# Kernel tuning notes

Hardware: AMD Instinct MI355X
Metric: run time of the kernel (lower is better)

## Reference

```python
import jax, jax.numpy as jnp
import numpy as np

N_HEAD = 16
MASK_NEG = -10000.0


def setup_inputs() -> dict:
    key = jax.random.key(0)
    k1, k2, k3 = jax.random.split(key, 3)
    B, S, D = 4, 2048, 1024
    x = jax.random.normal(k1, (B, S, D), dtype=jnp.float32)
    c_attn_w = jax.random.normal(k2, (D, 3 * D), dtype=jnp.float32) * 0.02
    c_attn_b = jnp.zeros((3 * D,), dtype=jnp.float32)
    c_proj_w = jax.random.normal(k3, (D, D), dtype=jnp.float32) * 0.02
    c_proj_b = jnp.zeros((D,), dtype=jnp.float32)
    return {"x": x, "c_attn_w": c_attn_w, "c_attn_b": c_attn_b,
            "c_proj_w": c_proj_w, "c_proj_b": c_proj_b}


def reference(x, c_attn_w, c_attn_b, c_proj_w, c_proj_b):
    B, S, D = x.shape
    H = N_HEAD
    Dh = D // H
    # fused QKV projection (Conv1D = x @ W + b)
    qkv = x @ c_attn_w + c_attn_b          # [B,S,3D]
    q, k, v = jnp.split(qkv, 3, axis=-1)   # each [B,S,D]
    # split heads -> [B,H,S,Dh]
    q = q.reshape(B, S, H, Dh).transpose(0, 2, 1, 3)
    k = k.reshape(B, S, H, Dh).transpose(0, 2, 1, 3)
    v = v.reshape(B, S, H, Dh).transpose(0, 2, 1, 3)
    # scores with scaling (scale=True)
    w = jnp.einsum('bhqd,bhkd->bhqk', q, k) / jnp.sqrt(jnp.float32(Dh))
    # multiplicative causal mask: w*b + -10000*(1-b)
    b = jnp.tril(jnp.ones((S, S), dtype=w.dtype))[None, None]  # [1,1,S,S]
    w = w * b + MASK_NEG * (1.0 - b)
    w = jax.nn.softmax(w, axis=-1)
    # dropout is identity at inference
    a = jnp.einsum('bhqk,bhkd->bhqd', w, v)  # [B,H,S,Dh]
    a = a.transpose(0, 2, 1, 3).reshape(B, S, D)  # merge heads
    out = a @ c_proj_w + c_proj_b
    return out
```

## Files before the change

### kernel.cpp

```cpp
#include <hip/hip_runtime.h>

typedef unsigned short u16;
typedef short bf16x8 __attribute__((ext_vector_type(8)));
typedef float f32x4 __attribute__((ext_vector_type(4)));
typedef unsigned int u32;
typedef u32 u32x4 __attribute__((ext_vector_type(4)));

#define B_ 4
#define S_ 2048
#define D_ 1024
#define H_ 16
#define DH_ 64
#define M_ 8192
#define SCL2E 0.1803368801111244f

__device__ __forceinline__ u16 f2b(float f) {
  union { float f; unsigned int u; } v; v.f = f;
  unsigned int u = v.u;
  unsigned int r = (u + 0x7FFFu + ((u >> 16) & 1u)) >> 16;
  return (u16)r;
}

__device__ __forceinline__ void gload16(const void* g, void* l) {
  __builtin_amdgcn_global_load_lds(
      (const __attribute__((address_space(1))) unsigned int*)g,
      (__attribute__((address_space(3))) unsigned int*)l,
      16, 0, 0);
}

__device__ __forceinline__ u32 cvt_pk_bf16(float lo, float hi) {
  u32 r;
  asm("v_cvt_pk_bf16_f32 %0, %1, %2" : "=v"(r) : "v"(lo), "v"(hi));
  return r;
}

struct __attribute__((aligned(8))) u16x4 { u16 x, y, z, w; };

__global__ void cvt_f32_bf16(const float* __restrict__ in, u16* __restrict__ out, int n) {
  int i = (blockIdx.x * blockDim.x + threadIdx.x) * 4;
  if (i >= n) return;
  float4 v = *(const float4*)(in + i);
  u16x4 o; o.x = f2b(v.x); o.y = f2b(v.y); o.z = f2b(v.z); o.w = f2b(v.w);
  *(u16x4*)(out + i) = o;
}

__global__ void transpose_cvt(const float* __restrict__ in, u16* __restrict__ out, int R, int C) {
  __shared__ float tile[32][33];
  int c0 = blockIdx.x * 32, r0 = blockIdx.y * 32;
  int tx = threadIdx.x, ty = threadIdx.y;
#pragma unroll
  for (int j = 0; j < 32; j += 8)
    tile[ty + j][tx] = in[(size_t)(r0 + ty + j) * C + c0 + tx];
  __syncthreads();
#pragma unroll
  for (int j = 0; j < 32; j += 8)
    out[(size_t)(c0 + ty + j) * R + r0 + tx] = f2b(tile[tx][ty + j]);
}

template <int MODE>
__global__ __launch_bounds__(256) void gemm_bt(
    const u16* __restrict__ A, const u16* __restrict__ BT,
    const float* __restrict__ bias, float* __restrict__ outf,
    u16* __restrict__ qb, u16* __restrict__ kb, u16* __restrict__ vtb,
    int Ncols, int Kdim) {
  __shared__ __attribute__((aligned(16))) u16 lsA[2][128 * 64];
  __shared__ __attribute__((aligned(16))) u16 lsB[2][128 * 64];
  const int t = threadIdx.x;
  const int lane = t & 63, w = t >> 6;
  const int lhi = lane >> 4, llo = lane & 15;

  const int gx = gridDim.x;
  const int lin = blockIdx.y * gx + blockIdx.x;
  const int nwg = gx * gridDim.y;
  const int sw = (lin & 7) * (nwg >> 3) + (lin >> 3);
  const int m0 = (sw / gx) * 128, n0 = (sw % gx) * 128;

  const int wr = (w >> 1) * 64, wc = (w & 1) * 64;

  const int r8 = lane >> 3;
  const int scolE = ((lane & 7) ^ r8) * 8;
  const int srow = w * 32 + r8;

  f32x4 acc[4][4] = {};
  const int nt = Kdim >> 6;

#define STAGE_G(buf, kk0)                                                        \
  _Pragma("unroll") for (int j = 0; j < 4; ++j) {                                \
    gload16(A + (size_t)(m0 + srow + j * 8) * Kdim + (kk0) + scolE,              \
            &lsA[buf][(w * 32 + j * 8) * 64]);                                   \
    gload16(BT + (size_t)(n0 + srow + j * 8) * Kdim + (kk0) + scolE,             \
            &lsB[buf][(w * 32 + j * 8) * 64]);                                   \
  }

  STAGE_G(0, 0)

  for (int tt = 0; tt < nt; ++tt) {
    const int cur = tt & 1;
    if (tt + 1 < nt) {
      STAGE_G(cur ^ 1, (tt + 1) << 6)
      asm volatile("s_waitcnt vmcnt(8)" ::: "memory");
    } else {
      asm volatile("s_waitcnt vmcnt(0)" ::: "memory");
    }
    __builtin_amdgcn_sched_barrier(0);
    __builtin_amdgcn_s_barrier();
    __builtin_amdgcn_sched_barrier(0);
#pragma unroll
    for (int kk = 0; kk < 2; ++kk) {
      bf16x8 af[4], bfr[4];
#pragma unroll
      for (int i = 0; i < 4; ++i) {
        int ra = wr + i * 16 + llo;
        af[i] = *(const bf16x8*)((const char*)&lsA[cur][ra * 64] +
                                 ((kk * 64 + lhi * 16) ^ ((ra & 7) << 4)));
        int rb = wc + i * 16 + llo;
        bfr[i] = *(const bf16x8*)((const char*)&lsB[cur][rb * 64] +
                                  ((kk * 64 + lhi * 16) ^ ((rb & 7) << 4)));
      }
#pragma unroll
      for (int mi = 0; mi < 4; ++mi)
#pragma unroll
        for (int ni = 0; ni < 4; ++ni)
          acc[mi][ni] = __builtin_amdgcn_mfma_f32_16x16x32_bf16(af[mi], bfr[ni], acc[mi][ni], 0, 0, 0);
    }
    __builtin_amdgcn_sched_barrier(0);
    __builtin_amdgcn_s_barrier();
  }
#undef STAGE_G

  if (MODE == 0) {
#pragma unroll
    for (int mi = 0; mi < 4; ++mi)
#pragma unroll
      for (int ni = 0; ni < 4; ++ni)
#pragma unroll
        for (int r = 0; r < 4; ++r) {
          int m = m0 + wr + mi * 16 + lhi * 4 + r;
          int n = n0 + wc + ni * 16 + llo;
          outf[(size_t)m * Ncols + n] = acc[mi][ni][r] + bias[n];
        }
  } else if (n0 < 1024) {
#pragma unroll
    for (int mi = 0; mi < 4; ++mi)
#pragma unroll
      for (int ni = 0; ni < 4; ++ni)
#pragma unroll
        for (int r = 0; r < 4; ++r) {
          int m = m0 + wr + mi * 16 + lhi * 4 + r;
          int n = n0 + wc + ni * 16 + llo;
          int bidx = m >> 11, s = m & 2047, hh = n >> 6, dh = n & 63;
          qb[((size_t)(bidx * 16 + hh) * 2048 + s) * 64 + dh] =
              f2b((acc[mi][ni][r] + bias[n]) * SCL2E);
        }
  } else if (n0 < 2048) {
#pragma unroll
    for (int mi = 0; mi < 4; ++mi)
#pragma unroll
      for (int ni = 0; ni < 4; ++ni)
#pragma unroll
        for (int r = 0; r < 4; ++r) {
          int m = m0 + wr + mi * 16 + lhi * 4 + r;
          int n2 = n0 - 1024 + wc + ni * 16 + llo;
          int bidx = m >> 11, s = m & 2047, hh = n2 >> 6, dh = n2 & 63;
          kb[((size_t)(bidx * 16 + hh) * 2048 + s) * 64 + dh] =
              f2b(acc[mi][ni][r] + bias[n0 + wc + ni * 16 + llo]);
        }
  } else {
#pragma unroll
    for (int mi = 0; mi < 4; ++mi)
#pragma unroll
      for (int ni = 0; ni < 4; ++ni)
#pragma unroll
        for (int r = 0; r < 4; ++r) {
          int m = m0 + wr + mi * 16 + lhi * 4 + r;
          int n2 = n0 - 2048 + wc + ni * 16 + llo;
          int bidx = m >> 11, s = m & 2047, hh = n2 >> 6, dh = n2 & 63;
          int col = (s & ~127) | ((s & 15) * 8 + ((s >> 4) & 7));
          vtb[((size_t)(bidx * 16 + hh) * 64 + dh) * 2048 + col] =
              f2b(acc[mi][ni][r] + bias[n0 + wc + ni * 16 + llo]);
        }
  }
}

__global__ __launch_bounds__(512) void attn128(
    const u16* __restrict__ Qb, const u16* __restrict__ Kb,
    const u16* __restrict__ VTb, u16* __restrict__ AO) {
  __shared__ __attribute__((aligned(16))) u16 kls[128 * 64];
  __shared__ __attribute__((aligned(16))) u16 vls[64 * 128];
  __shared__ __attribute__((aligned(16))) u16 pl[8][16][136];
  const int t = threadIdx.x, w = t >> 6, lane = t & 63;
  const int lhi = lane >> 4, llo = lane & 15;

  const int lin = blockIdx.y * 8 + blockIdx.x;
  const int bh = ((lin >> 6) << 3) | (lin & 7);
  const int pr = (lin >> 3) & 7;
  const int bb = bh >> 4, hh = bh & 15;

  const u16* Qp = Qb + (size_t)bh * (S_ * DH_);
  const u16* Kp = Kb + (size_t)bh * (S_ * DH_);
  const u16* Vp = VTb + (size_t)bh * (DH_ * S_);

  bf16x8 ones;
#pragma unroll
  for (int i = 0; i < 8; ++i) ones[i] = (short)0x3F80;

  int krow[2], kcolE[2], kdst[2], vrow[2], vcolE[2], vdst[2];
#pragma unroll
  for (int c = 0; c < 2; ++c) {
    int b = c * 8192 + t * 16;
    krow[c] = b >> 7;
    kcolE[c] = (b & 127) >> 1;
    kdst[c] = krow[c] * 128 + ((b & 127) ^ ((krow[c] & 7) << 4));
    vrow[c] = b >> 8;
    vcolE[c] = (b & 255) >> 1;
    vdst[c] = vrow[c] * 256 + ((b & 255) ^ ((vrow[c] & 15) << 4));
  }

  for (int ci = 0; ci < 2; ++ci) {
    const int qc = ci ? (15 - pr) : pr;
    const int q0 = qc * 128;
    const int qrow = q0 + w * 16 + llo;
    bf16x8 aq0 = *(const bf16x8*)(Qp + (size_t)qrow * DH_ + lhi * 8);
    bf16x8 aq1 = *(const bf16x8*)(Qp + (size_t)qrow * DH_ + 32 + lhi * 8);
    const int n128 = qc + 1;

    bf16x8 kst[2], vst[2];
#pragma unroll
    for (int c = 0; c < 2; ++c) {
      kst[c] = *(const bf16x8*)(Kp + (size_t)krow[c] * DH_ + kcolE[c]);
      vst[c] = *(const bf16x8*)(Vp + (size_t)vrow[c] * S_ + vcolE[c]);
    }
    __syncthreads();
#pragma unroll
    for (int c = 0; c < 2; ++c) {
      *(bf16x8*)((char*)kls + kdst[c]) = kst[c];
      *(bf16x8*)((char*)vls + vdst[c]) = vst[c];
    }
    __syncthreads();

    f32x4 o[4] = {};
    f32x4 osum = {};
    const int crow = q0 + w * 16 + lhi * 4;
    const int sw = (llo & 7) << 4;

    for (int tt = 0; tt < n128 - 1; ++tt) {
      const int kv0 = tt << 7;

#pragma unroll
      for (int c = 0; c < 2; ++c) {
        kst[c] = *(const bf16x8*)(Kp + (size_t)(kv0 + 128 + krow[c]) * DH_ + kcolE[c]);
        vst[c] = *(const bf16x8*)(Vp + (size_t)vrow[c] * S_ + kv0 + 128 + vcolE[c]);
      }

      f32x4 sc[8] = {};
      __builtin_amdgcn_s_setprio(1);
#pragma unroll
      for (int f = 0; f < 8; ++f) {
        const char* base = (const char*)kls + (f * 16 + llo) * 128;
        bf16x8 bk0 = *(const bf16x8*)(base + ((lhi * 16) ^ sw));
        bf16x8 bk1 = *(const bf16x8*)(base + ((64 + lhi * 16) ^ sw));
        sc[f] = __builtin_amdgcn_mfma_f32_16x16x32_bf16(aq0, bk0, sc[f], 0, 0, 0);
        sc[f] = __builtin_amdgcn_mfma_f32_16x16x32_bf16(aq1, bk1, sc[f], 0, 0, 0);
      }
      __builtin_amdgcn_s_setprio(0);

#pragma unroll
      for (int r = 0; r < 4; ++r) {
        float p[8];
#pragma unroll
        for (int f = 0; f < 8; ++f) p[f] = exp2f(sc[f][r]);
        u32x4 pw;
        pw[0] = cvt_pk_bf16(p[0], p[1]);
        pw[1] = cvt_pk_bf16(p[2], p[3]);
        pw[2] = cvt_pk_bf16(p[4], p[5]);
        pw[3] = cvt_pk_bf16(p[6], p[7]);
        *(u32x4*)((char*)&pl[w][lhi * 4 + r][0] + llo * 16) = pw;
      }

      __builtin_amdgcn_s_setprio(1);
#pragma unroll
      for (int kk = 0; kk < 4; ++kk) {
        bf16x8 ap = *(const bf16x8*)((const char*)&pl[w][llo][0] + kk * 64 + lhi * 16);
#pragma unroll
        for (int f = 0; f < 4; ++f) {
          const char* vbase = (const char*)vls + (f * 16 + llo) * 256;
          bf16x8 bv = *(const bf16x8*)(vbase + ((kk * 64 + lhi * 16) ^ (llo << 4)));
          o[f] = __builtin_amdgcn_mfma_f32_16x16x32_bf16(ap, bv, o[f], 0, 0, 0);
        }
        osum = __builtin_amdgcn_mfma_f32_16x16x32_bf16(ap, ones, osum, 0, 0, 0);
      }
      __builtin_amdgcn_s_setprio(0);

      __syncthreads();
#pragma unroll
      for (int c = 0; c < 2; ++c) {
        *(bf16x8*)((char*)kls + kdst[c]) = kst[c];
        *(bf16x8*)((char*)vls + vdst[c]) = vst[c];
      }
      __syncthreads();
    }

    {
      const int kv0 = (n128 - 1) << 7;
      f32x4 sc[8] = {};
      __builtin_amdgcn_s_setprio(1);
#pragma unroll
      for (int f = 0; f < 8; ++f) {
        const char* base = (const char*)kls + (f * 16 + llo) * 128;
        bf16x8 bk0 = *(const bf16x8*)(base + ((lhi * 16) ^ sw));
        bf16x8 bk1 = *(const bf16x8*)(base + ((64 + lhi * 16) ^ sw));
        sc[f] = __builtin_amdgcn_mfma_f32_16x16x32_bf16(aq0, bk0, sc[f], 0, 0, 0);
        sc[f] = __builtin_amdgcn_mfma_f32_16x16x32_bf16(aq1, bk1, sc[f], 0, 0, 0);
      }
      __builtin_amdgcn_s_setprio(0);

#pragma unroll
      for (int r = 0; r < 4; ++r) {
        float p[8];
#pragma unroll
        for (int f = 0; f < 8; ++f) {
          float x = sc[f][r];
          if (kv0 + f * 16 + llo > crow + r) x = -1e30f;
          p[f] = exp2f(x);
        }
        u32x4 pw;
        pw[0] = cvt_pk_bf16(p[0], p[1]);
        pw[1] = cvt_pk_bf16(p[2], p[3]);
        pw[2] = cvt_pk_bf16(p[4], p[5]);
        pw[3] = cvt_pk_bf16(p[6], p[7]);
        *(u32x4*)((char*)&pl[w][lhi * 4 + r][0] + llo * 16) = pw;
      }

      __builtin_amdgcn_s_setprio(1);
#pragma unroll
      for (int kk = 0; kk < 4; ++kk) {
        bf16x8 ap = *(const bf16x8*)((const char*)&pl[w][llo][0] + kk * 64 + lhi * 16);
#pragma unroll
        for (int f = 0; f < 4; ++f) {
          const char* vbase = (const char*)vls + (f * 16 + llo) * 256;
          bf16x8 bv = *(const bf16x8*)(vbase + ((kk * 64 + lhi * 16) ^ (llo << 4)));
          o[f] = __builtin_amdgcn_mfma_f32_16x16x32_bf16(ap, bv, o[f], 0, 0, 0);
        }
        osum = __builtin_amdgcn_mfma_f32_16x16x32_bf16(ap, ones, osum, 0, 0, 0);
      }
      __builtin_amdgcn_s_setprio(0);
    }

#pragma unroll
    for (int f = 0; f < 4; ++f)
#pragma unroll
      for (int r = 0; r < 4; ++r) {
        int row = crow + r;
        int dh = f * 16 + llo;
        float val = o[f][r] / osum[r];
        AO[((size_t)bb * S_ + row) * D_ + hh * DH_ + dh] = f2b(val);
      }
  }
}

extern "C" void kernel_launch(void* const* d_in, const int* in_sizes, int n_in,
                              void* d_out, int out_size, void* d_ws, size_t ws_size,
                              hipStream_t stream) {
  const float* x  = (const float*)d_in[0];
  const float* w1 = (const float*)d_in[1];
  const float* b1 = (const float*)d_in[2];
  const float* w2 = (const float*)d_in[3];
  const float* b2 = (const float*)d_in[4];
  float* out = (float*)d_out;
  char* ws = (char*)d_ws;

  u16* xb  = (u16*)(ws);
  u16* w1t = (u16*)(ws + 16777216);
  u16* w2t = (u16*)(ws + 23068672);
  u16* qb  = (u16*)(ws + 25165824);
  u16* kb  = (u16*)(ws + 41943040);
  u16* vtb = (u16*)(ws + 58720256);
  u16* ao  = xb;

  cvt_f32_bf16<<<8192, 256, 0, stream>>>(x, xb, M_ * D_);
  transpose_cvt<<<dim3(96, 32), dim3(32, 8), 0, stream>>>(w1, w1t, 1024, 3072);
  transpose_cvt<<<dim3(32, 32), dim3(32, 8), 0, stream>>>(w2, w2t, 1024, 1024);

  gemm_bt<1><<<dim3(24, 64), 256, 0, stream>>>(xb, w1t, b1, nullptr, qb, kb, vtb, 3072, 1024);
  attn128<<<dim3(8, 64), 512, 0, stream>>>(qb, kb, vtb, ao);
  gemm_bt<0><<<dim3(8, 64), 256, 0, stream>>>(ao, w2t, b2, out, nullptr, nullptr, nullptr, 1024, 1024);
}
```

Measured before the change: 185.5 us.

## Replace QKV GEMM with 256x256-tile 8-wave kernel with phased LDS pipelining

Adds a new gemm256 kernel for the QKV projection that uses 256x256 output tiles with 512 threads, double-buffered LDS, and a four-phase schedule interleaving global-to-LDS loads with MFMA work. Workgroup indices are swizzled across XCD-sized groups for L2 locality. The aim is higher arithmetic intensity and better overlap of memory traffic with compute than the 128x128 gemm_bt path. In exchange, the grid shrinks to 384 blocks at one block per CU, which may leave some CUs idle or unbalanced and raises register pressure.

```diff
diff --git a/kernel.cpp b/kernel.cpp
--- a/kernel.cpp
+++ b/kernel.cpp
@@ -139,45 +139,137 @@
           int n = n0 + wc + ni * 16 + llo;
           outf[(size_t)m * Ncols + n] = acc[mi][ni][r] + bias[n];
         }
-  } else if (n0 < 1024) {
-#pragma unroll
-    for (int mi = 0; mi < 4; ++mi)
-#pragma unroll
-      for (int ni = 0; ni < 4; ++ni)
+  }
+}
+
+__global__ __launch_bounds__(512, 1) void gemm256(
+    const u16* __restrict__ A, const u16* __restrict__ BT,
+    const float* __restrict__ bias,
+    u16* __restrict__ qb, u16* __restrict__ kb, u16* __restrict__ vtb,
+    int Kdim) {
+  __shared__ __attribute__((aligned(16))) u16 lsA[2][2][128 * 64];
+  __shared__ __attribute__((aligned(16))) u16 lsB[2][2][128 * 64];
+  const int t = threadIdx.x;
+  const int lane = t & 63, w = t >> 6;
+  const int lhi = lane >> 4, llo = lane & 15;
+
+  const int gx = gridDim.x;
+  const int lin = blockIdx.y * gx + blockIdx.x;
+  const int nwg = gx * gridDim.y;
+  const int sw = (lin & 7) * (nwg >> 3) + (lin >> 3);
+  const int m0 = (sw / gx) * 256, n0 = (sw % gx) * 256;
+
+  const int wr = w >> 2, wc = w & 3;
+  const int srowj = t >> 3;
+  const int scol = ((t & 7) ^ (srowj & 7)) * 8;
+  const u16* gA = A + (size_t)m0 * Kdim;
+  const u16* gB = BT + (size_t)n0 * Kdim;
+
+  f32x4 acc[8][4] = {};
+  const int nt = Kdim >> 6;
+
+#define STG256(buf, h, kk0)                                                     \
+  { const u16* gp = ((h) < 2 ? gA + (size_t)((h) * 128) * Kdim                  \
+                             : gB + (size_t)(((h) - 2) * 128) * Kdim);          \
+    u16* lp = ((h) < 2 ? &lsA[buf][(h)][0] : &lsB[buf][(h) - 2][0]);            \
+    _Pragma("unroll") for (int j = 0; j < 2; ++j)                               \
+      gload16(gp + (size_t)(j * 64 + srowj) * Kdim + (kk0) + scol,              \
+              lp + j * 4096 + w * 512); }
+
+  STG256(0, 0, 0) STG256(0, 1, 0) STG256(0, 2, 0) STG256(0, 3, 0)
+
+  bf16x8 af[4][2], bfr[2][2];
+
+#define RDA256(c, mh)                                                            \
+  _Pragma("unroll") for (int mi = 0; mi < 4; ++mi)                               \
+  _Pragma("unroll") for (int kk = 0; kk < 2; ++kk) {                             \
+    int rih = (mh) * 64 + mi * 16 + llo;                                         \
+    af[mi][kk] = *(const bf16x8*)((const char*)&lsA[c][wr][0] + rih * 128 +      \
+                                  ((kk * 64 + lhi * 16) ^ ((rih & 7) << 4)));    \
+  }
+#define RDB256(c, nh)                                                            \
+  _Pragma("unroll") for (int ni = 0; ni < 2; ++ni)                               \
+  _Pragma("unroll") for (int kk = 0; kk < 2; ++kk) {                             \
+    int rih = (wc & 1) * 64 + (nh) * 32 + ni * 16 + llo;                         \
+    bfr[ni][kk] = *(const bf16x8*)((const char*)&lsB[c][wc >> 1][0] + rih * 128 +\
+                                   ((kk * 64 + lhi * 16) ^ ((rih & 7) << 4)));   \
+  }
+#define MFMA256(mh, nh)                                                          \
+  __builtin_amdgcn_s_setprio(1);                                                 \
+  _Pragma("unroll") for (int kk = 0; kk < 2; ++kk)                               \
+  _Pragma("unroll") for (int mi = 0; mi < 4; ++mi)                               \
+  _Pragma("unroll") for (int ni = 0; ni < 2; ++ni)                               \
+    acc[(mh) * 4 + mi][(nh) * 2 + ni] = __builtin_amdgcn_mfma_f32_16x16x32_bf16( \
+        af[mi][kk], bfr[ni][kk], acc[(mh) * 4 + mi][(nh) * 2 + ni], 0, 0, 0);    \
+  __builtin_amdgcn_s_setprio(0);
+#define PH_SYNC(cnt)                                                             \
+  asm volatile("s_waitcnt vmcnt(" #cnt ")" ::: "memory");                        \
+  __builtin_amdgcn_sched_barrier(0);                                             \
+  __builtin_amdgcn_s_barrier();                                                  \
+  __builtin_amdgcn_sched_barrier(0);
+
+  for (int kt = 0; kt < nt - 1; ++kt) {
+    const int c = kt & 1, o = c ^ 1;
+    const int kn = (kt + 1) << 6;
+    PH_SYNC(6) RDA256(c, 0) RDB256(c, 0) STG256(o, 0, kn) MFMA256(0, 0)
+    PH_SYNC(6) RDB256(c, 1)              STG256(o, 1, kn) MFMA256(0, 1)
+    PH_SYNC(6) RDA256(c, 1)              STG256(o, 2, kn) MFMA256(1, 1)
+    PH_SYNC(6) RDB256(c, 0)              STG256(o, 3, kn) MFMA256(1, 0)
+  }
+  {
+    const int c = (nt - 1) & 1;
+    PH_SYNC(6) RDA256(c, 0) RDB256(c, 0) MFMA256(0, 0)
+    PH_SYNC(4) RDB256(c, 1)              MFMA256(0, 1)
+    PH_SYNC(2) RDA256(c, 1)              MFMA256(1, 1)
+    PH_SYNC(0) RDB256(c, 0)              MFMA256(1, 0)
+  }
+#undef STG256
+#undef RDA256
+#undef RDB256
+#undef MFMA256
+#undef PH_SYNC
+
+  if (n0 < 1024) {
+#pragma unroll
+    for (int MI = 0; MI < 8; ++MI)
+#pragma unroll
+      for (int NI = 0; NI < 4; ++NI)
 #pragma unroll
         for (int r = 0; r < 4; ++r) {
-          int m = m0 + wr + mi * 16 + lhi * 4 + r;
-          int n = n0 + wc + ni * 16 + llo;
+          int m = m0 + wr * 128 + MI * 16 + lhi * 4 + r;
+          int n = n0 + wc * 64 + NI * 16 + llo;
           int bidx = m >> 11, s = m & 2047, hh = n >> 6, dh = n & 63;
           qb[((size_t)(bidx * 16 + hh) * 2048 + s) * 64 + dh] =
-              f2b((acc[mi][ni][r] + bias[n]) * SCL2E);
+              f2b((acc[MI][NI][r] + bias[n]) * SCL2E);
         }
   } else if (n0 < 2048) {
 #pragma unroll
-    for (int mi = 0; mi < 4; ++mi)
-#pragma unroll
-      for (int ni = 0; ni < 4; ++ni)
+    for (int MI = 0; MI < 8; ++MI)
+#pragma unroll
+      for (int NI = 0; NI < 4; ++NI)
 #pragma unroll
         for (int r = 0; r < 4; ++r) {
-          int m = m0 + wr + mi * 16 + lhi * 4 + r;
-          int n2 = n0 - 1024 + wc + ni * 16 + llo;
+          int m = m0 + wr * 128 + MI * 16 + lhi * 4 + r;
+          int n = n0 + wc * 64 + NI * 16 + llo;
+          int n2 = n - 1024;
           int bidx = m >> 11, s = m & 2047, hh = n2 >> 6, dh = n2 & 63;
           kb[((size_t)(bidx * 16 + hh) * 2048 + s) * 64 + dh] =
-              f2b(acc[mi][ni][r] + bias[n0 + wc + ni * 16 + llo]);
+              f2b(acc[MI][NI][r] + bias[n]);
         }
   } else {
 #pragma unroll
-    for (int mi = 0; mi < 4; ++mi)
-#pragma unroll
-      for (int ni = 0; ni < 4; ++ni)
+    for (int MI = 0; MI < 8; ++MI)
+#pragma unroll
+      for (int NI = 0; NI < 4; ++NI)
 #pragma unroll
         for (int r = 0; r < 4; ++r) {
-          int m = m0 + wr + mi * 16 + lhi * 4 + r;
-          int n2 = n0 - 2048 + wc + ni * 16 + llo;
+          int m = m0 + wr * 128 + MI * 16 + lhi * 4 + r;
+          int n = n0 + wc * 64 + NI * 16 + llo;
+          int n2 = n - 2048;
           int bidx = m >> 11, s = m & 2047, hh = n2 >> 6, dh = n2 & 63;
           int col = (s & ~127) | ((s & 15) * 8 + ((s >> 4) & 7));
           vtb[((size_t)(bidx * 16 + hh) * 64 + dh) * 2048 + col] =
-              f2b(acc[mi][ni][r] + bias[n0 + wc + ni * 16 + llo]);
+              f2b(acc[MI][NI][r] + bias[n]);
         }
   }
 }
@@ -245,7 +337,6 @@
 
     for (int tt = 0; tt < n128 - 1; ++tt) {
       const int kv0 = tt << 7;
-
 #pragma unroll
       for (int c = 0; c < 2; ++c) {
         kst[c] = *(const bf16x8*)(Kp + (size_t)(kv0 + 128 + krow[c]) * DH_ + kcolE[c]);
@@ -381,7 +472,7 @@
   transpose_cvt<<<dim3(96, 32), dim3(32, 8), 0, stream>>>(w1, w1t, 1024, 3072);
   transpose_cvt<<<dim3(32, 32), dim3(32, 8), 0, stream>>>(w2, w2t, 1024, 1024);
 
-  gemm_bt<1><<<dim3(24, 64), 256, 0, stream>>>(xb, w1t, b1, nullptr, qb, kb, vtb, 3072, 1024);
+  gemm256<<<dim3(12, 32), 512, 0, stream>>>(xb, w1t, b1, qb, kb, vtb, 1024);
   attn128<<<dim3(8, 64), 512, 0, stream>>>(qb, kb, vtb, ao);
   gemm_bt<0><<<dim3(8, 64), 256, 0, stream>>>(ao, w2t, b2, out, nullptr, nullptr, nullptr, 1024, 1024);
 }
```

Result: slower. 211.8 us (+14.1%).
